# Optimization experiments

Hardware: AMD Instinct MI355X
Metric: run time of the kernel (lower is better)

## Reference

```python
import jax, jax.numpy as jnp
import numpy as np


def setup_inputs() -> dict:
    key = jax.random.key(0)
    ks = jax.random.split(key, 8)
    B, C, H, W = 16, 192, 64, 64
    dt_rank, d_state = 12, 1
    return {
        "x": jax.random.normal(ks[0], (B, C, H, W), dtype=jnp.float32),
        "conv_w": jax.random.normal(ks[1], (C, 1, 5, 5), dtype=jnp.float32) * 0.1,
        "conv_b": jax.random.normal(ks[2], (C,), dtype=jnp.float32) * 0.1,
        "x_proj_w": jax.random.normal(ks[3], (dt_rank + 2 * d_state, C), dtype=jnp.float32) * (C ** -0.5),
        "dt_w": jax.random.normal(ks[4], (C, dt_rank), dtype=jnp.float32) * (dt_rank ** -0.5),
        "dt_b": jax.random.normal(ks[5], (C,), dtype=jnp.float32) * 0.1,
        "A_logs": jnp.zeros((C, d_state), dtype=jnp.float32),  # log(arange(1,d_state+1)) with d_state=1 -> 0
        "Ds": jnp.ones((C,), dtype=jnp.float32),
    }


def reference(x, conv_w, conv_b, x_proj_w, dt_w, dt_b, A_logs, Ds):
    B, C, H, W = x.shape
    L = H * W
    dt_rank = dt_w.shape[1]
    n = A_logs.shape[1]  # d_state
    # depthwise conv2d, kernel 5, padding SAME (=d_conv//2), then SiLU
    x = jax.lax.conv_general_dilated(
        x, conv_w, window_strides=(1, 1), padding='SAME',
        feature_group_count=C, dimension_numbers=('NCHW', 'OIHW', 'NCHW'))
    x = jax.nn.silu(x + conv_b[None, :, None, None])
    xs = x.reshape(B, C, L)  # (b, d, l)
    # x_proj: (dt_rank + 2n, C) @ (b, C, l)
    x_dbl = jnp.einsum('kc,bcl->bkl', x_proj_w, xs)
    dts, Bs, Cs = jnp.split(x_dbl, [dt_rank, dt_rank + n], axis=1)
    # dt projection + softplus (delta_softplus=True with delta_bias)
    delta = jax.nn.softplus(jnp.einsum('cr,brl->bcl', dt_w, dts) + dt_b[None, :, None])  # (b,d,l)
    A = -jnp.exp(A_logs)  # (d, n)
    # selective scan returning the full state trajectory h_t (b,d,n,l):
    # h_t = exp(delta_t * A) * h_{t-1} + delta_t * B_t * u_t
    a = jnp.exp(delta[:, :, None, :] * A[None, :, :, None])        # (b,d,n,l)
    b_el = delta[:, :, None, :] * Bs[:, None, :, :] * xs[:, :, None, :]  # (b,d,n,l)

    def combine(e1, e2):
        a1, b1 = e1
        a2, b2 = e2
        return (a1 * a2, a2 * b1 + b2)

    _, h = jax.lax.associative_scan(combine, (a, b_el), axis=-1)  # h: (b,d,n,l)
    state = h.reshape(B, C * n, L)
    # y = C_t * h_t + D * u (fp32, d_state=1 broadcast)
    y = state.astype(jnp.float32) * Cs.astype(jnp.float32) + xs * Ds[:, None]
    return y.reshape(B, C, H, W)
```

## Files before the change

### kernel.cpp

```cpp
#include <hip/hip_runtime.h>
#include <hip/hip_bf16.h>
#include <cstddef>

#define BB 16
#define CC 192
#define HH 64
#define WW 64
#define LL 4096
#define DTR 12
#define KK 14

__device__ __forceinline__ float silu_f(float v) {
  return v / (1.f + __expf(-v));
}

__global__ __launch_bounds__(256) void conv_silu_kernel(
    const float* __restrict__ x, const float* __restrict__ cw,
    const float* __restrict__ cb, float* __restrict__ xs) {
  const int bc = blockIdx.x;
  const int c = bc % CC;
  const int tid = threadIdx.x;
  const int lane = tid & 63;
  const int wv = tid >> 6;
  const int oy0 = wv * 16;

  float w[25];
#pragma unroll
  for (int k = 0; k < 25; ++k) w[k] = cw[c * 25 + k];
  const float bias = cb[c];

  const float* xp = x + (size_t)bc * LL + lane;
  float* op = xs + (size_t)bc * LL + lane;

  float rv[20];
#pragma unroll
  for (int r = 0; r < 20; ++r) {
    const int gr = oy0 + r - 2;
    float v = 0.f;
    if ((unsigned)gr < 64u) v = xp[gr * 64];
    rv[r] = v;
  }

  float acc[5];
#pragma unroll
  for (int i = 0; i < 5; ++i) acc[i] = 0.f;

#pragma unroll
  for (int r = 0; r < 20; ++r) {
    float v = rv[r];
    float vm2 = __shfl_up(v, 2u, 64);
    float vm1 = __shfl_up(v, 1u, 64);
    float vp1 = __shfl_down(v, 1u, 64);
    float vp2 = __shfl_down(v, 2u, 64);
    if (lane < 2) vm2 = 0.f;
    if (lane < 1) vm1 = 0.f;
    if (lane > 62) vp1 = 0.f;
    if (lane > 61) vp2 = 0.f;
    float t[5] = {vm2, vm1, v, vp1, vp2};
#pragma unroll
    for (int ky = 0; ky < 5; ++ky) {
      if (r >= ky && (r - ky) < 16) {
        float s = acc[(r - ky) % 5];
#pragma unroll
        for (int kx = 0; kx < 5; ++kx) s += w[ky * 5 + kx] * t[kx];
        acc[(r - ky) % 5] = s;
      }
    }
    if (r >= 4) {
      const int yf = oy0 + r - 4;
      float a = acc[(r - 4) % 5] + bias;
      op[yf * 64] = silu_f(a);
      acc[(r - 4) % 5] = 0.f;
    }
  }
}

__global__ __launch_bounds__(512) void projdt_kernel(
    const float* __restrict__ xs, const float* __restrict__ xpw,
    const float* __restrict__ dtw, const float* __restrict__ dtb,
    float* __restrict__ delta, float* __restrict__ Bsp,
    float* __restrict__ Csp) {
  const int b = blockIdx.y;
  const int l0 = blockIdx.x * 128;
  const int tid = threadIdx.x;
  const int lane = tid & 63;
  const int g = tid >> 6;

  __shared__ float part[8][KK][132];

  float2 acc[KK];
#pragma unroll
  for (int k = 0; k < KK; ++k) acc[k] = make_float2(0.f, 0.f);

  const float* bp = xs + ((size_t)(b * CC + g * 24)) * LL + l0 + lane * 2;
#pragma unroll 4
  for (int cc = 0; cc < 24; ++cc) {
    float2 v = *(const float2*)(bp + (size_t)cc * LL);
    const int c = g * 24 + cc;
#pragma unroll
    for (int k = 0; k < KK; ++k) {
      float wv = xpw[k * CC + c];
      acc[k].x += wv * v.x;
      acc[k].y += wv * v.y;
    }
  }
#pragma unroll
  for (int k = 0; k < KK; ++k)
    *(float2*)&part[g][k][lane * 2] = acc[k];
  __syncthreads();

  const int l = tid & 127;
  const int cg = tid >> 7;
  float dts[DTR];
#pragma unroll
  for (int r = 0; r < DTR; ++r) {
    float v = 0.f;
#pragma unroll
    for (int p = 0; p < 8; ++p) v += part[p][r][l];
    dts[r] = v;
  }
  if (cg == 3) {
    float vb = 0.f, vc = 0.f;
#pragma unroll
    for (int p = 0; p < 8; ++p) {
      vb += part[p][12][l];
      vc += part[p][13][l];
    }
    Bsp[(size_t)b * LL + l0 + l] = vb;
    Csp[(size_t)b * LL + l0 + l] = vc;
  }

  float* dp = delta + ((size_t)b * CC + cg * 48) * LL + l0 + l;
  for (int i = 0; i < 48; ++i) {
    const int c = cg * 48 + i;
    float z = dtb[c];
#pragma unroll
    for (int r = 0; r < DTR; ++r) z += dtw[c * DTR + r] * dts[r];
    float d = (z > 15.f) ? z : __logf(1.f + __expf(z));
    dp[(size_t)i * LL] = d;
  }
}

__global__ __launch_bounds__(256) void scan_kernel(
    const float* __restrict__ xs, const float* __restrict__ delta,
    const float* __restrict__ Bsp, const float* __restrict__ Csp,
    const float* __restrict__ A_logs, const float* __restrict__ Ds,
    float* __restrict__ y) {
  const int bc = blockIdx.x;
  const int b = bc / CC;
  const int c = bc - b * CC;
  const int tid = threadIdx.x;
  const int lane = tid & 63;
  const int wv = tid >> 6;

  const float Ac = -__expf(A_logs[c]);
  const float Dc = Ds[c];

  const float* xp = xs + (size_t)bc * LL;
  const float* ddp = delta + (size_t)bc * LL;
  const float* bpp = Bsp + (size_t)b * LL;
  const float* cpp = Csp + (size_t)b * LL;
  float* yp = y + (size_t)bc * LL;

  __shared__ float segA[4];
  __shared__ float segB[4];

  float PA = 1.f;
  float hB = 0.f;
  float u[16], v[16];

#pragma unroll
  for (int ck = 0; ck < 4; ++ck) {
    const int base = wv * 1024 + ck * 256 + lane * 4;
    const float4 x4 = *(const float4*)(xp + base);
    const float4 d4 = *(const float4*)(ddp + base);
    const float4 B4 = *(const float4*)(bpp + base);
    const float4 C4 = *(const float4*)(cpp + base);

    float av[4], bv[4];
    float aggA = 1.f, aggB = 0.f;
#pragma unroll
    for (int q = 0; q < 4; ++q) {
      const float dl = (&d4.x)[q];
      float a = __expf(dl * Ac);
      float be = dl * ((&B4.x)[q]) * ((&x4.x)[q]);
      av[q] = a;
      bv[q] = be;
      aggA = a * aggA;
      aggB = a * aggB + be;
    }

    float incA = aggA, incB = aggB;
#pragma unroll
    for (int s = 1; s < 64; s <<= 1) {
      float pA = __shfl_up(incA, (unsigned)s, 64);
      float pB = __shfl_up(incB, (unsigned)s, 64);
      if (lane >= s) {
        incB = incA * pB + incB;
        incA = incA * pA;
      }
    }
    float eA = __shfl_up(incA, 1u, 64);
    float eB = __shfl_up(incB, 1u, 64);
    if (lane == 0) { eA = 1.f; eB = 0.f; }
    const float tA = __shfl(incA, 63, 64);
    const float tB = __shfl(incB, 63, 64);

    float h = eA * hB + eB;
    float P = PA * eA;
#pragma unroll
    for (int q = 0; q < 4; ++q) {
      h = av[q] * h + bv[q];
      P = P * av[q];
      u[ck * 4 + q] = P * ((&C4.x)[q]);
      v[ck * 4 + q] = h * ((&C4.x)[q]) + ((&x4.x)[q]) * Dc;
    }

    hB = tA * hB + tB;
    PA = PA * tA;
  }

  if (lane == 0) { segA[wv] = PA; segB[wv] = hB; }
  __syncthreads();

  float carry = 0.f;
  for (int i = 0; i < wv; ++i) carry = segA[i] * carry + segB[i];

#pragma unroll
  for (int ck = 0; ck < 4; ++ck) {
    const int base = wv * 1024 + ck * 256 + lane * 4;
    float4 o;
    o.x = u[ck * 4 + 0] * carry + v[ck * 4 + 0];
    o.y = u[ck * 4 + 1] * carry + v[ck * 4 + 1];
    o.z = u[ck * 4 + 2] * carry + v[ck * 4 + 2];
    o.w = u[ck * 4 + 3] * carry + v[ck * 4 + 3];
    *(float4*)(yp + base) = o;
  }
}

extern "C" void kernel_launch(void* const* d_in, const int* in_sizes, int n_in,
                              void* d_out, int out_size, void* d_ws,
                              size_t ws_size, hipStream_t stream) {
  const float* x        = (const float*)d_in[0];
  const float* conv_w   = (const float*)d_in[1];
  const float* conv_b   = (const float*)d_in[2];
  const float* x_proj_w = (const float*)d_in[3];
  const float* dt_w     = (const float*)d_in[4];
  const float* dt_b     = (const float*)d_in[5];
  const float* A_logs   = (const float*)d_in[6];
  const float* Ds       = (const float*)d_in[7];
  float* out = (float*)d_out;

  char* ws = (char*)d_ws;
  const size_t plane_bytes = (size_t)BB * CC * LL * sizeof(float);
  const size_t bl_bytes    = (size_t)BB * LL * sizeof(float);
  float* xs    = (float*)ws;
  float* delta = (float*)(ws + plane_bytes);
  float* Bsp   = (float*)(ws + 2 * plane_bytes);
  float* Csp   = (float*)(ws + 2 * plane_bytes + bl_bytes);

  conv_silu_kernel<<<dim3(BB * CC), 256, 0, stream>>>(x, conv_w, conv_b, xs);
  projdt_kernel<<<dim3(LL / 128, BB), 512, 0, stream>>>(
      xs, x_proj_w, dt_w, dt_b, delta, Bsp, Csp);
  scan_kernel<<<dim3(BB * CC), 256, 0, stream>>>(xs, delta, Bsp, Csp,
                                                 A_logs, Ds, out);
}
```

Measured before the change: 174.0 us.

## Fuse depthwise conv+SiLU into projection/dt kernel, reduce partials via LDS atomics

```diff
diff --git a/kernel.cpp b/kernel.cpp
--- a/kernel.cpp
+++ b/kernel.cpp
@@ -14,122 +14,91 @@
   return v / (1.f + __expf(-v));
 }
 
-__global__ __launch_bounds__(256) void conv_silu_kernel(
+__global__ __launch_bounds__(512) void convprojdt_kernel(
     const float* __restrict__ x, const float* __restrict__ cw,
-    const float* __restrict__ cb, float* __restrict__ xs) {
-  const int bc = blockIdx.x;
-  const int c = bc % CC;
-  const int tid = threadIdx.x;
-  const int lane = tid & 63;
-  const int wv = tid >> 6;
-  const int oy0 = wv * 16;
-
-  float w[25];
-#pragma unroll
-  for (int k = 0; k < 25; ++k) w[k] = cw[c * 25 + k];
-  const float bias = cb[c];
-
-  const float* xp = x + (size_t)bc * LL + lane;
-  float* op = xs + (size_t)bc * LL + lane;
-
-  float rv[20];
-#pragma unroll
-  for (int r = 0; r < 20; ++r) {
-    const int gr = oy0 + r - 2;
-    float v = 0.f;
-    if ((unsigned)gr < 64u) v = xp[gr * 64];
-    rv[r] = v;
-  }
-
-  float acc[5];
-#pragma unroll
-  for (int i = 0; i < 5; ++i) acc[i] = 0.f;
-
-#pragma unroll
-  for (int r = 0; r < 20; ++r) {
-    float v = rv[r];
-    float vm2 = __shfl_up(v, 2u, 64);
-    float vm1 = __shfl_up(v, 1u, 64);
-    float vp1 = __shfl_down(v, 1u, 64);
-    float vp2 = __shfl_down(v, 2u, 64);
-    if (lane < 2) vm2 = 0.f;
-    if (lane < 1) vm1 = 0.f;
-    if (lane > 62) vp1 = 0.f;
-    if (lane > 61) vp2 = 0.f;
-    float t[5] = {vm2, vm1, v, vp1, vp2};
-#pragma unroll
-    for (int ky = 0; ky < 5; ++ky) {
-      if (r >= ky && (r - ky) < 16) {
-        float s = acc[(r - ky) % 5];
-#pragma unroll
-        for (int kx = 0; kx < 5; ++kx) s += w[ky * 5 + kx] * t[kx];
-        acc[(r - ky) % 5] = s;
-      }
-    }
-    if (r >= 4) {
-      const int yf = oy0 + r - 4;
-      float a = acc[(r - 4) % 5] + bias;
-      op[yf * 64] = silu_f(a);
-      acc[(r - 4) % 5] = 0.f;
-    }
-  }
-}
-
-__global__ __launch_bounds__(512) void projdt_kernel(
-    const float* __restrict__ xs, const float* __restrict__ xpw,
+    const float* __restrict__ cb, const float* __restrict__ xpw,
     const float* __restrict__ dtw, const float* __restrict__ dtb,
-    float* __restrict__ delta, float* __restrict__ Bsp,
-    float* __restrict__ Csp) {
+    float* __restrict__ xs, float* __restrict__ delta,
+    float* __restrict__ Bsp, float* __restrict__ Csp) {
   const int b = blockIdx.y;
-  const int l0 = blockIdx.x * 128;
+  const int s = blockIdx.x;
+  const int l0 = s * 128;
+  const int y0 = s * 2;
   const int tid = threadIdx.x;
   const int lane = tid & 63;
   const int g = tid >> 6;
 
-  __shared__ float part[8][KK][132];
+  __shared__ float dts_lds[KK][128];
+  for (int i = tid; i < KK * 128; i += 512) ((float*)dts_lds)[i] = 0.f;
+  __syncthreads();
 
   float2 acc[KK];
 #pragma unroll
   for (int k = 0; k < KK; ++k) acc[k] = make_float2(0.f, 0.f);
 
-  const float* bp = xs + ((size_t)(b * CC + g * 24)) * LL + l0 + lane * 2;
-#pragma unroll 4
+  const int c0 = g * 24;
+#pragma unroll 2
   for (int cc = 0; cc < 24; ++cc) {
-    float2 v = *(const float2*)(bp + (size_t)cc * LL);
-    const int c = g * 24 + cc;
+    const int c = c0 + cc;
+    const float* xpp = x + ((size_t)(b * CC + c)) * LL + lane;
+    float r[6];
+#pragma unroll
+    for (int j = 0; j < 6; ++j) {
+      const int gy = y0 - 2 + j;
+      r[j] = ((unsigned)gy < 64u) ? xpp[gy * 64] : 0.f;
+    }
+    float s0 = cb[c], s1 = cb[c];
+#pragma unroll
+    for (int j = 0; j < 6; ++j) {
+      float v = r[j];
+      float vm2 = __shfl_up(v, 2u, 64);
+      float vm1 = __shfl_up(v, 1u, 64);
+      float vp1 = __shfl_down(v, 1u, 64);
+      float vp2 = __shfl_down(v, 2u, 64);
+      if (lane < 2) vm2 = 0.f;
+      if (lane < 1) vm1 = 0.f;
+      if (lane > 62) vp1 = 0.f;
+      if (lane > 61) vp2 = 0.f;
+      float t[5] = {vm2, vm1, v, vp1, vp2};
+      if (j < 5) {
+#pragma unroll
+        for (int kx = 0; kx < 5; ++kx) s0 += cw[c * 25 + j * 5 + kx] * t[kx];
+      }
+      if (j >= 1) {
+#pragma unroll
+        for (int kx = 0; kx < 5; ++kx)
+          s1 += cw[c * 25 + (j - 1) * 5 + kx] * t[kx];
+      }
+    }
+    const float v0 = silu_f(s0);
+    const float v1 = silu_f(s1);
+    float* xsp = xs + ((size_t)(b * CC + c)) * LL + l0 + lane;
+    xsp[0] = v0;
+    xsp[64] = v1;
 #pragma unroll
     for (int k = 0; k < KK; ++k) {
-      float wv = xpw[k * CC + c];
-      acc[k].x += wv * v.x;
-      acc[k].y += wv * v.y;
-    }
-  }
-#pragma unroll
-  for (int k = 0; k < KK; ++k)
-    *(float2*)&part[g][k][lane * 2] = acc[k];
+      const float wv = xpw[k * CC + c];
+      acc[k].x += wv * v0;
+      acc[k].y += wv * v1;
+    }
+  }
+
+#pragma unroll
+  for (int k = 0; k < KK; ++k) {
+    atomicAdd(&dts_lds[k][lane], acc[k].x);
+    atomicAdd(&dts_lds[k][64 + lane], acc[k].y);
+  }
   __syncthreads();
 
   const int l = tid & 127;
   const int cg = tid >> 7;
   float dts[DTR];
 #pragma unroll
-  for (int r = 0; r < DTR; ++r) {
-    float v = 0.f;
-#pragma unroll
-    for (int p = 0; p < 8; ++p) v += part[p][r][l];
-    dts[r] = v;
-  }
+  for (int r = 0; r < DTR; ++r) dts[r] = dts_lds[r][l];
   if (cg == 3) {
-    float vb = 0.f, vc = 0.f;
-#pragma unroll
-    for (int p = 0; p < 8; ++p) {
-      vb += part[p][12][l];
-      vc += part[p][13][l];
-    }
-    Bsp[(size_t)b * LL + l0 + l] = vb;
-    Csp[(size_t)b * LL + l0 + l] = vc;
-  }
-
+    Bsp[(size_t)b * LL + l0 + l] = dts_lds[12][l];
+    Csp[(size_t)b * LL + l0 + l] = dts_lds[13][l];
+  }
   float* dp = delta + ((size_t)b * CC + cg * 48) * LL + l0 + l;
   for (int i = 0; i < 48; ++i) {
     const int c = cg * 48 + i;
@@ -192,10 +161,10 @@
 
     float incA = aggA, incB = aggB;
 #pragma unroll
-    for (int s = 1; s < 64; s <<= 1) {
-      float pA = __shfl_up(incA, (unsigned)s, 64);
-      float pB = __shfl_up(incB, (unsigned)s, 64);
-      if (lane >= s) {
+    for (int st = 1; st < 64; st <<= 1) {
+      float pA = __shfl_up(incA, (unsigned)st, 64);
+      float pB = __shfl_up(incB, (unsigned)st, 64);
+      if (lane >= st) {
         incB = incA * pB + incB;
         incA = incA * pA;
       }
@@ -259,9 +228,8 @@
   float* Bsp   = (float*)(ws + 2 * plane_bytes);
   float* Csp   = (float*)(ws + 2 * plane_bytes + bl_bytes);
 
-  conv_silu_kernel<<<dim3(BB * CC), 256, 0, stream>>>(x, conv_w, conv_b, xs);
-  projdt_kernel<<<dim3(LL / 128, BB), 512, 0, stream>>>(
-      xs, x_proj_w, dt_w, dt_b, delta, Bsp, Csp);
+  convprojdt_kernel<<<dim3(LL / 128, BB), 512, 0, stream>>>(
+      x, conv_w, conv_b, x_proj_w, dt_w, dt_b, xs, delta, Bsp, Csp);
   scan_kernel<<<dim3(BB * CC), 256, 0, stream>>>(xs, delta, Bsp, Csp,
                                                  A_logs, Ds, out);
 }
```

Result: slower. 224.2 us (+28.8%).
